# Kernel tuning notes

Hardware: AMD Instinct MI355X
Metric: run time of the kernel (lower is better)

The kernel has to match this reference:

```python
import jax, jax.numpy as jnp
import numpy as np

DIM = 768
N_HEAD = 12
HEAD_DIM = 64
INNER = N_HEAD * HEAD_DIM
SCALE = HEAD_DIM ** -0.5


def setup_inputs() -> dict:
    key = jax.random.key(0)
    ks = jax.random.split(key, 12)
    B, Sf, St = 4, 2048, 2048
    from_tensor = jax.random.normal(ks[0], (B, Sf, DIM), dtype=jnp.float32)
    to_tensor = jax.random.normal(ks[1], (B, St, DIM), dtype=jnp.float32)
    attention_mask = jax.random.randint(ks[2], (B, Sf, St), 0, 2, dtype=jnp.int32)
    # Dense layers: kernel ~ RandomNormal (stddev 0.05, keras default), bias zeros
    def kern(k, fan_in, fan_out):
        return 0.05 * jax.random.normal(k, (fan_in, fan_out), dtype=jnp.float32)
    return {
        "from_tensor": from_tensor,
        "to_tensor": to_tensor,
        "attention_mask": attention_mask,
        "Wq": kern(ks[3], DIM, INNER), "bq": jnp.zeros((INNER,), jnp.float32),
        "Wk": kern(ks[4], DIM, INNER), "bk": jnp.zeros((INNER,), jnp.float32),
        "Wv": kern(ks[5], DIM, INNER), "bv": jnp.zeros((INNER,), jnp.float32),
        "Wo": kern(ks[6], INNER, DIM), "bo": jnp.zeros((DIM,), jnp.float32),
    }


def reference(from_tensor, to_tensor, attention_mask, Wq, bq, Wk, bk, Wv, bv, Wo, bo):
    B, Sf, _ = from_tensor.shape
    St = to_tensor.shape[1]
    # projections -> [B, S, n_head, head_dim] -> [B, n_head, S, head_dim]
    def split_heads(x, S):
        return x.reshape(B, S, N_HEAD, HEAD_DIM).transpose(0, 2, 1, 3)
    q = split_heads(from_tensor @ Wq + bq, Sf) * SCALE
    k = split_heads(to_tensor @ Wk + bk, St)
    v = split_heads(to_tensor @ Wv + bv, St)
    # scores [B, H, Sf, St]
    scores = jnp.einsum('bhik,bhjk->bhij', q, k)
    adder = (1.0 - attention_mask.astype(jnp.float32)) * -10000.0
    scores = scores + adder[:, None, :, :]
    probs = jax.nn.softmax(scores, axis=-1)
    out = jnp.einsum('bhij,bhjk->bhik', probs, v)  # [B, H, Sf, Dh]
    out = out.transpose(0, 2, 1, 3).reshape(B, Sf, INNER)
    return out @ Wo + bo
```

## Files before the change

### kernel.cpp

```cpp
#include <hip/hip_runtime.h>
#include <stdint.h>

#define DIM 768
#define NH 12
#define HD 64
#define BSZ 4
#define SEQ 2048
#define MROWS (BSZ*SEQ)

typedef __attribute__((ext_vector_type(8))) short v8s;
typedef __attribute__((ext_vector_type(4))) float v4f;
typedef __attribute__((ext_vector_type(8))) _Float16 v8h;
typedef __attribute__((ext_vector_type(2))) __fp16 v2fp;

__device__ __forceinline__ uint16_t f2bf(float x) {
  union { float f; uint32_t u; } v; v.f = x;
  uint32_t r = v.u + 0x7fffu + ((v.u >> 16) & 1u);
  return (uint16_t)(r >> 16);
}

#if __has_builtin(__builtin_amdgcn_cvt_pk_bf16_f32)
typedef __attribute__((ext_vector_type(2))) __bf16 v2bf;
__device__ __forceinline__ uint32_t pack_bf16(float a, float b) {
  union { v2bf v; uint32_t u; } c;
  c.v = __builtin_amdgcn_cvt_pk_bf16_f32(a, b);
  return c.u;
}
#else
__device__ __forceinline__ uint32_t pack_bf16(float a, float b) {
  return (uint32_t)f2bf(a) | ((uint32_t)f2bf(b) << 16);
}
#endif

__device__ __forceinline__ uint32_t pack_f16(float a, float b) {
#if __has_builtin(__builtin_amdgcn_cvt_pkrtz)
  union { v2fp h; uint32_t u; } c;
  c.h = __builtin_amdgcn_cvt_pkrtz(a, b);
  return c.u;
#else
  union { _Float16 h[2]; uint32_t u; } c;
  c.h[0] = (_Float16)a; c.h[1] = (_Float16)b; return c.u;
#endif
}

__device__ __forceinline__ float fexp2(float x) {
#if __has_builtin(__builtin_amdgcn_exp2f)
  return __builtin_amdgcn_exp2f(x);
#else
  return exp2f(x);
#endif
}

__device__ __forceinline__ void gl16(const void* g, void* l) {
  __builtin_amdgcn_global_load_lds(
      (const __attribute__((address_space(1))) unsigned int*)g,
      (__attribute__((address_space(3))) unsigned int*)l, 16, 0, 0);
}

__device__ __forceinline__ void pipe_sync() {
  asm volatile("s_waitcnt vmcnt(0)" ::: "memory");
  __builtin_amdgcn_s_barrier();
  __builtin_amdgcn_sched_barrier(0);
}

__global__ void cvt_bf16_kernel(const float* __restrict__ src0, uint16_t* __restrict__ dst0,
                                const float* __restrict__ src1, uint16_t* __restrict__ dst1,
                                int n4) {
  int i = blockIdx.x * blockDim.x + threadIdx.x;
  const float* src = (i < n4) ? src0 : src1;
  uint16_t* dst = (i < n4) ? dst0 : dst1;
  int j = (i < n4) ? i : i - n4;
  float4 v = ((const float4*)src)[j];
  ushort4 o;
  o.x = f2bf(v.x); o.y = f2bf(v.y); o.z = f2bf(v.z); o.w = f2bf(v.w);
  ((ushort4*)dst)[j] = o;
}

__global__ void mask_bits_kernel(const int* __restrict__ src,
                                 unsigned long long* __restrict__ dst, int nwords) {
  int gtid = blockIdx.x * blockDim.x + threadIdx.x;
  int w = gtid >> 6;
  int lane = threadIdx.x & 63;
  if (w >= nwords) return;
  int b  = w >> 16;
  int q  = (w >> 5) & 2047;
  int kt = w & 31;
  int m = src[((size_t)b * SEQ + q) * SEQ + kt * 64 + lane];
  unsigned long long bits = __ballot(m != 0);
  if (lane == 0) dst[((size_t)b * 32 + kt) * SEQ + q] = bits;
}

__global__ void wtrans_kernel(const float* __restrict__ Wq, const float* __restrict__ Wk,
                              const float* __restrict__ Wv, const float* __restrict__ Wo,
                              uint16_t* __restrict__ WT) {
  __shared__ float tile[32][33];
  int z = blockIdx.z;
  const float* src = (z==0) ? Wq : (z==1) ? Wk : (z==2) ? Wv : Wo;
  uint16_t* dst = WT + (size_t)z * DIM * DIM;
  int tx = threadIdx.x, ty = threadIdx.y;
  int x  = blockIdx.x * 32 + tx;
  int y0 = blockIdx.y * 32;
  for (int j = ty; j < 32; j += 8)
    tile[j][tx] = src[(size_t)(y0 + j) * DIM + x];
  __syncthreads();
  int xo = y0 + tx;
  for (int j = ty; j < 32; j += 8)
    dst[(size_t)(blockIdx.x * 32 + j) * DIM + xo] = f2bf(tile[tx][j]);
}

__global__ __launch_bounds__(256) void gemm_kernel(
    const uint16_t* __restrict__ Xf, const uint16_t* __restrict__ Xt,
    const uint16_t* __restrict__ WT, const uint16_t* __restrict__ AO,
    const float* __restrict__ bq, const float* __restrict__ bk,
    const float* __restrict__ bv, const float* __restrict__ bo,
    uint16_t* __restrict__ Qw, uint16_t* __restrict__ Kw, uint16_t* __restrict__ Vw,
    float* __restrict__ Out, int mode_base)
{
  __shared__ alignas(16) uint16_t As[2][128 * 32];
  __shared__ alignas(16) uint16_t Bs[2][128 * 32];
  int mode = mode_base + blockIdx.z;
  const uint16_t* A = (mode == 0) ? Xf : (mode == 3 ? AO : Xt);
  const uint16_t* W = WT + (size_t)mode * DIM * DIM;
  const float* bias = (mode == 0) ? bq : (mode == 1) ? bk : (mode == 2) ? bv : bo;

  int m0 = blockIdx.x * 128, n0 = blockIdx.y * 128;
  int tid = threadIdx.x;
  int wave = tid >> 6, lane = tid & 63, lr = lane & 15, quad = lane >> 4;
  int wm = (wave >> 1) * 64, wn = (wave & 1) * 64;

  int seg = (lane & 3) ^ ((lane >> 3) & 3);
  const uint16_t* agl = A + (size_t)(m0 + wave * 32 + (lane >> 2)) * DIM + seg * 8;
  const uint16_t* bgl = W + (size_t)(n0 + wave * 32 + (lane >> 2)) * DIM + seg * 8;
  int lb = wave * 1024;
  int ck = (lr >> 1) & 3;

  v4f acc[4][4];
  v4f vz = {0.f, 0.f, 0.f, 0.f};
  #pragma unroll
  for (int i = 0; i < 4; i++)
    #pragma unroll
    for (int j = 0; j < 4; j++) acc[i][j] = vz;

  gl16(agl,            &As[0][lb]);
  gl16(agl + 16 * DIM, &As[0][lb + 512]);
  gl16(bgl,            &Bs[0][lb]);
  gl16(bgl + 16 * DIM, &Bs[0][lb + 512]);
  pipe_sync();

  int cur = 0;
  const int NT = DIM / 32;
  for (int t = 0; t < NT; ++t) {
    if (t + 1 < NT) {
      int kn = (t + 1) * 32;
      gl16(agl + kn,            &As[cur ^ 1][lb]);
      gl16(agl + kn + 16 * DIM, &As[cur ^ 1][lb + 512]);
      gl16(bgl + kn,            &Bs[cur ^ 1][lb]);
      gl16(bgl + kn + 16 * DIM, &Bs[cur ^ 1][lb + 512]);
    }
    v8s af[4], bfr[4];
    #pragma unroll
    for (int i = 0; i < 4; i++)
      af[i] = *(const v8s*)&As[cur][(wm + i * 16 + lr) * 32 + ((quad ^ ck) << 3)];
    #pragma unroll
    for (int j = 0; j < 4; j++)
      bfr[j] = *(const v8s*)&Bs[cur][(wn + j * 16 + lr) * 32 + ((quad ^ ck) << 3)];
    #pragma unroll
    for (int i = 0; i < 4; i++)
      #pragma unroll
      for (int j = 0; j < 4; j++)
        acc[i][j] = __builtin_amdgcn_mfma_f32_16x16x32_bf16(af[i], bfr[j], acc[i][j], 0, 0, 0);
    if (t + 1 < NT) pipe_sync();
    cur ^= 1;
  }

  float bj[4];
  #pragma unroll
  for (int j = 0; j < 4; j++) bj[j] = bias[n0 + wn + j * 16 + lr];

  if (mode == 3) {
    #pragma unroll
    for (int i = 0; i < 4; i++) {
      int m = m0 + wm + i * 16 + quad * 4;
      #pragma unroll
      for (int j = 0; j < 4; j++) {
        int n = n0 + wn + j * 16 + lr;
        #pragma unroll
        for (int r = 0; r < 4; r++)
          Out[(size_t)(m + r) * DIM + n] = acc[i][j][r] + bj[j];
      }
    }
  } else if (mode == 2) {
    #pragma unroll
    for (int i = 0; i < 4; i++) {
      int m = m0 + wm + i * 16 + quad * 4;
      int b = m >> 11, s0 = m & 2047;
      int kk0 = s0 & 63;
      int pos = (kk0 >> 5) * 32 + ((kk0 >> 2) & 3) * 8 + ((kk0 >> 4) & 1) * 4;
      int chunk = pos >> 3, off = pos & 7;
      #pragma unroll
      for (int j = 0; j < 4; j++) {
        int n = n0 + wn + j * 16 + lr;
        int h = n >> 6, d = n & 63;
        uint2 pk;
        pk.x = pack_f16(acc[i][j][0] + bj[j], acc[i][j][1] + bj[j]);
        pk.y = pack_f16(acc[i][j][2] + bj[j], acc[i][j][3] + bj[j]);
        int idx = (s0 & ~63) + ((chunk ^ (d & 7)) << 3) + off;
        *(uint2*)&Vw[((size_t)(b * NH + h) * HD + d) * SEQ + idx] = pk;
      }
    }
  } else {
    uint16_t* Dst = (mode == 0) ? Qw : Kw;
    float scale = (mode == 0) ? 0.18033688f : 1.0f;
    #pragma unroll
    for (int i = 0; i < 4; i++) {
      int m = m0 + wm + i * 16 + quad * 4;
      int b = m >> 11, s0 = m & 2047;
      #pragma unroll
      for (int j = 0; j < 4; j++) {
        int n = n0 + wn + j * 16 + lr;
        int h = n >> 6, d = n & 63;
        #pragma unroll
        for (int r = 0; r < 4; r++) {
          float v = (acc[i][j][r] + bj[j]) * scale;
          int s = s0 + r;
          int dd = (mode == 1) ? ((((d >> 3) ^ (s & 7)) << 3) + (d & 7)) : d;
          Dst[((size_t)(b * NH + h) * SEQ + s) * HD + dd] = f2bf(v);
        }
      }
    }
  }
}

__global__ __launch_bounds__(512, 6) void flash_kernel(
    const uint16_t* __restrict__ Qg, const uint16_t* __restrict__ Kg,
    const uint16_t* __restrict__ Vg, const unsigned long long* __restrict__ Mb,
    uint16_t* __restrict__ AO)
{
  __shared__ alignas(16) uint16_t Ks[2][64 * 64];
  __shared__ alignas(16) uint16_t Vs[2][64 * 64];

  int tid = threadIdx.x, wave = tid >> 6, lane = tid & 63, lr = lane & 15, quad = lane >> 4;

  int d = blockIdx.x + (blockIdx.y << 4);
  int nid = (d & 7) * 96 + (d >> 3);
  int bh = nid >> 4;
  int q0 = (nid & 15) * 128;
  int b = bh / NH, h = bh - b * NH;

  const uint16_t* Qp = Qg + (size_t)bh * SEQ * HD;
  const uint16_t* Kp = Kg + (size_t)bh * SEQ * HD;
  const uint16_t* Vp = Vg + (size_t)bh * HD * SEQ;
  int qg = q0 + wave * 16 + lr;
  const unsigned long long* Mp = Mb + (size_t)b * 32 * SEQ + qg;

  int swk = lr & 7, sh0 = quad * 4;

  v8s qfa = *(const v8s*)&Qp[(size_t)qg * HD + quad * 8];
  v8s qfb = *(const v8s*)&Qp[(size_t)qg * HD + 32 + quad * 8];

  const uint16_t* kgl = Kp + ((size_t)(wave * 8 + (lane >> 3)) * HD + (lane & 7) * 8);
  const uint16_t* vgl = Vp + ((size_t)(wave * 8 + (lane >> 3)) * SEQ + (lane & 7) * 8);
  int lb = wave * 512;

  v8h ones;
  #pragma unroll
  for (int i = 0; i < 8; i++) ones[i] = (_Float16)1.0f;

  v4f acc[4], lacc;
  v4f vz = {0.f, 0.f, 0.f, 0.f};
  v4f m8 = {-8.f, -8.f, -8.f, -8.f};
  #pragma unroll
  for (int dt = 0; dt < 4; dt++) acc[dt] = vz;
  lacc = vz;

  gl16(kgl, &Ks[0][lb]);
  gl16(vgl, &Vs[0][lb]);
  unsigned long long mw_cur = Mp[0];
  __syncthreads();

  int cur = 0;
  const int NT = SEQ / 64;
  for (int it = 0; it < NT; ++it) {
    unsigned long long mw_next = 0;
    if (it + 1 < NT) {
      int kn = (it + 1) * 64;
      gl16(kgl + (size_t)kn * HD, &Ks[cur ^ 1][lb]);
      gl16(vgl + kn,              &Vs[cur ^ 1][lb]);
      mw_next = Mp[(size_t)(it + 1) * SEQ];
    }

    uint32_t mlo = (uint32_t)mw_cur, mhi = (uint32_t)(mw_cur >> 32);
    v8h pf[2];
    #pragma unroll
    for (int p = 0; p < 2; p++) {
      v4f sA = m8, sB = m8;
      {
        int rowb = ((2 * p) * 16 + lr) << 6;
        v8s kf0 = *(const v8s*)&Ks[cur][rowb + ((quad ^ swk) << 3)];
        v8s kf1 = *(const v8s*)&Ks[cur][rowb + (((quad + 4) ^ swk) << 3)];
        sA = __builtin_amdgcn_mfma_f32_16x16x32_bf16(kf0, qfa, sA, 0, 0, 0);
        sA = __builtin_amdgcn_mfma_f32_16x16x32_bf16(kf1, qfb, sA, 0, 0, 0);
      }
      {
        int rowb = ((2 * p + 1) * 16 + lr) << 6;
        v8s kf0 = *(const v8s*)&Ks[cur][rowb + ((quad ^ swk) << 3)];
        v8s kf1 = *(const v8s*)&Ks[cur][rowb + (((quad + 4) ^ swk) << 3)];
        sB = __builtin_amdgcn_mfma_f32_16x16x32_bf16(kf0, qfa, sB, 0, 0, 0);
        sB = __builtin_amdgcn_mfma_f32_16x16x32_bf16(kf1, qfb, sB, 0, 0, 0);
      }
      uint32_t mword = p ? mhi : mlo;
      uint32_t b4a = (mword >> sh0) & 15u;
      uint32_t b4b = (mword >> (sh0 + 16)) & 15u;
      float ps[8];
      #pragma unroll
      for (int r = 0; r < 4; r++) {
        float ea = fexp2(sA[r]);
        float eb = fexp2(sB[r]);
        ps[r]     = (b4a & (1u << r)) ? ea : 0.0f;
        ps[4 + r] = (b4b & (1u << r)) ? eb : 0.0f;
      }
      union { uint4 u; v8h h; } cc;
      cc.u.x = pack_f16(ps[0], ps[1]);
      cc.u.y = pack_f16(ps[2], ps[3]);
      cc.u.z = pack_f16(ps[4], ps[5]);
      cc.u.w = pack_f16(ps[6], ps[7]);
      pf[p] = cc.h;
    }

    #pragma unroll
    for (int dt = 0; dt < 4; dt++) {
      int rowb = (dt * 16 + lr) << 6;
      #pragma unroll
      for (int p = 0; p < 2; p++) {
        v8h vv = *(const v8h*)&Vs[cur][rowb + (((p * 4 + quad) ^ swk) << 3)];
        acc[dt] = __builtin_amdgcn_mfma_f32_16x16x32_f16(vv, pf[p], acc[dt], 0, 0, 0);
      }
    }
    lacc = __builtin_amdgcn_mfma_f32_16x16x32_f16(ones, pf[0], lacc, 0, 0, 0);
    lacc = __builtin_amdgcn_mfma_f32_16x16x32_f16(ones, pf[1], lacc, 0, 0, 0);

    __syncthreads();
    mw_cur = mw_next;
    cur ^= 1;
  }

  float ri = 1.0f / lacc[0];

  #pragma unroll
  for (int dt = 0; dt < 4; dt++) {
    uint2 pk;
    pk.x = pack_bf16(acc[dt][0] * ri, acc[dt][1] * ri);
    pk.y = pack_bf16(acc[dt][2] * ri, acc[dt][3] * ri);
    *(uint2*)&AO[(size_t)(b * SEQ + qg) * DIM + h * HD + dt * 16 + sh0] = pk;
  }
}

extern "C" void kernel_launch(void* const* d_in, const int* in_sizes, int n_in,
                              void* d_out, int out_size, void* d_ws, size_t ws_size,
                              hipStream_t stream) {
  const float* from_t = (const float*)d_in[0];
  const float* to_t   = (const float*)d_in[1];
  const int*   maski  = (const int*)d_in[2];
  const float* Wq = (const float*)d_in[3];  const float* bq = (const float*)d_in[4];
  const float* Wk = (const float*)d_in[5];  const float* bk = (const float*)d_in[6];
  const float* Wv = (const float*)d_in[7];  const float* bv = (const float*)d_in[8];
  const float* Wo = (const float*)d_in[9];  const float* bo = (const float*)d_in[10];

  char* ws = (char*)d_ws;
  size_t off = 0;
  uint16_t* Xf = (uint16_t*)(ws + off); off += (size_t)MROWS * DIM * 2;
  uint16_t* Xt = (uint16_t*)(ws + off); off += (size_t)MROWS * DIM * 2;
  uint16_t* WT = (uint16_t*)(ws + off); off += (size_t)4 * DIM * DIM * 2;
  unsigned long long* Mbits = (unsigned long long*)(ws + off);
  off += (size_t)BSZ * 32 * SEQ * 8;
  uint16_t* Qw = (uint16_t*)(ws + off); off += (size_t)MROWS * DIM * 2;
  uint16_t* Kw = (uint16_t*)(ws + off); off += (size_t)MROWS * DIM * 2;
  uint16_t* Vw = (uint16_t*)(ws + off); off += (size_t)MROWS * DIM * 2;
  uint16_t* AO = (uint16_t*)(ws + off); off += (size_t)MROWS * DIM * 2;
  float* Out = (float*)d_out;

  int nx4 = MROWS * DIM / 4;
  cvt_bf16_kernel<<<2 * nx4 / 256, 256, 0, stream>>>(from_t, Xf, to_t, Xt, nx4);
  int nwords = BSZ * 32 * SEQ;
  mask_bits_kernel<<<nwords * 64 / 256, 256, 0, stream>>>(maski, Mbits, nwords);
  wtrans_kernel<<<dim3(24, 24, 4), dim3(32, 8), 0, stream>>>(Wq, Wk, Wv, Wo, WT);

  gemm_kernel<<<dim3(64, 6, 3), 256, 0, stream>>>(Xf, Xt, WT, AO, bq, bk, bv, bo,
                                                  Qw, Kw, Vw, Out, 0);
  flash_kernel<<<dim3(SEQ / 128, BSZ * NH), 512, 0, stream>>>(Qw, Kw, Vw, Mbits, AO);
  gemm_kernel<<<dim3(64, 6, 1), 256, 0, stream>>>(Xf, Xt, WT, AO, bq, bk, bv, bo,
                                                  Qw, Kw, Vw, Out, 3);
}
```

Measured before the change: 328.1 us.

## Fuse prepass kernels into one launch and vectorize GEMM epilogue stores via operand swap

Merges the bf16 conversion, mask bit-packing and weight transpose kernels into a single prepass launch dispatched by block index, which removes two kernel launches and the gaps between them. In the GEMM, the Q/K and output modes swap the MFMA operands so each lane holds four consecutive columns. This lets the epilogue write packed 8-byte bf16 or 16-byte float4 stores and read the bias as a float4, instead of issuing scalar strided stores. The V mode keeps the old operand order and its existing transposed layout.

```diff
diff --git a/kernel.cpp b/kernel.cpp
--- a/kernel.cpp
+++ b/kernel.cpp
@@ -63,49 +63,56 @@
   __builtin_amdgcn_sched_barrier(0);
 }
 
-__global__ void cvt_bf16_kernel(const float* __restrict__ src0, uint16_t* __restrict__ dst0,
-                                const float* __restrict__ src1, uint16_t* __restrict__ dst1,
-                                int n4) {
-  int i = blockIdx.x * blockDim.x + threadIdx.x;
-  const float* src = (i < n4) ? src0 : src1;
-  uint16_t* dst = (i < n4) ? dst0 : dst1;
-  int j = (i < n4) ? i : i - n4;
-  float4 v = ((const float4*)src)[j];
-  ushort4 o;
-  o.x = f2bf(v.x); o.y = f2bf(v.y); o.z = f2bf(v.z); o.w = f2bf(v.w);
-  ((ushort4*)dst)[j] = o;
-}
-
-__global__ void mask_bits_kernel(const int* __restrict__ src,
-                                 unsigned long long* __restrict__ dst, int nwords) {
-  int gtid = blockIdx.x * blockDim.x + threadIdx.x;
-  int w = gtid >> 6;
-  int lane = threadIdx.x & 63;
-  if (w >= nwords) return;
-  int b  = w >> 16;
-  int q  = (w >> 5) & 2047;
-  int kt = w & 31;
-  int m = src[((size_t)b * SEQ + q) * SEQ + kt * 64 + lane];
-  unsigned long long bits = __ballot(m != 0);
-  if (lane == 0) dst[((size_t)b * 32 + kt) * SEQ + q] = bits;
-}
-
-__global__ void wtrans_kernel(const float* __restrict__ Wq, const float* __restrict__ Wk,
-                              const float* __restrict__ Wv, const float* __restrict__ Wo,
-                              uint16_t* __restrict__ WT) {
+#define CVT_BLKS  12288
+#define MASK_BLKS 65536
+#define WT_BLKS   2304
+__global__ __launch_bounds__(256) void prepass_kernel(
+    const float* __restrict__ from_t, const float* __restrict__ to_t,
+    uint16_t* __restrict__ Xf, uint16_t* __restrict__ Xt,
+    const int* __restrict__ maski, unsigned long long* __restrict__ Mbits,
+    const float* __restrict__ Wq, const float* __restrict__ Wk,
+    const float* __restrict__ Wv, const float* __restrict__ Wo,
+    uint16_t* __restrict__ WT)
+{
   __shared__ float tile[32][33];
-  int z = blockIdx.z;
-  const float* src = (z==0) ? Wq : (z==1) ? Wk : (z==2) ? Wv : Wo;
-  uint16_t* dst = WT + (size_t)z * DIM * DIM;
-  int tx = threadIdx.x, ty = threadIdx.y;
-  int x  = blockIdx.x * 32 + tx;
-  int y0 = blockIdx.y * 32;
-  for (int j = ty; j < 32; j += 8)
-    tile[j][tx] = src[(size_t)(y0 + j) * DIM + x];
-  __syncthreads();
-  int xo = y0 + tx;
-  for (int j = ty; j < 32; j += 8)
-    dst[(size_t)(blockIdx.x * 32 + j) * DIM + xo] = f2bf(tile[tx][j]);
+  int blk = blockIdx.x, tid = threadIdx.x;
+  if (blk < CVT_BLKS) {
+    int n4 = MROWS * DIM / 4;
+    int i = blk * 256 + tid;
+    const float* src = (i < n4) ? from_t : to_t;
+    uint16_t* dst = (i < n4) ? Xf : Xt;
+    int j = (i < n4) ? i : i - n4;
+    float4 v = ((const float4*)src)[j];
+    uint2 o;
+    o.x = pack_bf16(v.x, v.y);
+    o.y = pack_bf16(v.z, v.w);
+    ((uint2*)dst)[j] = o;
+  } else if (blk < CVT_BLKS + MASK_BLKS) {
+    int gtid = (blk - CVT_BLKS) * 256 + tid;
+    int w = gtid >> 6;
+    int lane = tid & 63;
+    int b  = w >> 16;
+    int q  = (w >> 5) & 2047;
+    int kt = w & 31;
+    int m = maski[((size_t)b * SEQ + q) * SEQ + kt * 64 + lane];
+    unsigned long long bits = __ballot(m != 0);
+    if (lane == 0) Mbits[((size_t)b * 32 + kt) * SEQ + q] = bits;
+  } else {
+    int r = blk - CVT_BLKS - MASK_BLKS;
+    int z = r / 576, rem = r - z * 576;
+    int by = rem / 24, bx = rem - by * 24;
+    const float* src = (z==0) ? Wq : (z==1) ? Wk : (z==2) ? Wv : Wo;
+    uint16_t* dst = WT + (size_t)z * DIM * DIM;
+    int tx = tid & 31, ty = tid >> 5;
+    int x  = bx * 32 + tx;
+    int y0 = by * 32;
+    for (int jj = ty; jj < 32; jj += 8)
+      tile[jj][tx] = src[(size_t)(y0 + jj) * DIM + x];
+    __syncthreads();
+    int xo = y0 + tx;
+    for (int jj = ty; jj < 32; jj += 8)
+      dst[(size_t)(bx * 32 + jj) * DIM + xo] = f2bf(tile[tx][jj]);
+  }
 }
 
 __global__ __launch_bounds__(256) void gemm_kernel(
@@ -164,32 +171,27 @@
     #pragma unroll
     for (int j = 0; j < 4; j++)
       bfr[j] = *(const v8s*)&Bs[cur][(wn + j * 16 + lr) * 32 + ((quad ^ ck) << 3)];
-    #pragma unroll
-    for (int i = 0; i < 4; i++)
-      #pragma unroll
-      for (int j = 0; j < 4; j++)
-        acc[i][j] = __builtin_amdgcn_mfma_f32_16x16x32_bf16(af[i], bfr[j], acc[i][j], 0, 0, 0);
+    if (mode != 2) {
+      #pragma unroll
+      for (int i = 0; i < 4; i++)
+        #pragma unroll
+        for (int j = 0; j < 4; j++)
+          acc[i][j] = __builtin_amdgcn_mfma_f32_16x16x32_bf16(bfr[j], af[i], acc[i][j], 0, 0, 0);
+    } else {
+      #pragma unroll
+      for (int i = 0; i < 4; i++)
+        #pragma unroll
+        for (int j = 0; j < 4; j++)
+          acc[i][j] = __builtin_amdgcn_mfma_f32_16x16x32_bf16(af[i], bfr[j], acc[i][j], 0, 0, 0);
+    }
     if (t + 1 < NT) pipe_sync();
     cur ^= 1;
   }
 
-  float bj[4];
-  #pragma unroll
-  for (int j = 0; j < 4; j++) bj[j] = bias[n0 + wn + j * 16 + lr];
-
-  if (mode == 3) {
-    #pragma unroll
-    for (int i = 0; i < 4; i++) {
-      int m = m0 + wm + i * 16 + quad * 4;
-      #pragma unroll
-      for (int j = 0; j < 4; j++) {
-        int n = n0 + wn + j * 16 + lr;
-        #pragma unroll
-        for (int r = 0; r < 4; r++)
-          Out[(size_t)(m + r) * DIM + n] = acc[i][j][r] + bj[j];
-      }
-    }
-  } else if (mode == 2) {
+  if (mode == 2) {
+    float bj[4];
+    #pragma unroll
+    for (int j = 0; j < 4; j++) bj[j] = bias[n0 + wn + j * 16 + lr];
     #pragma unroll
     for (int i = 0; i < 4; i++) {
       int m = m0 + wm + i * 16 + quad * 4;
@@ -208,24 +210,43 @@
         *(uint2*)&Vw[((size_t)(b * NH + h) * HD + d) * SEQ + idx] = pk;
       }
     }
+  } else if (mode == 3) {
+    #pragma unroll
+    for (int j = 0; j < 4; j++) {
+      int nb = n0 + wn + j * 16 + quad * 4;
+      float4 b4 = *(const float4*)&bias[nb];
+      #pragma unroll
+      for (int i = 0; i < 4; i++) {
+        int m = m0 + wm + i * 16 + lr;
+        float4 o;
+        o.x = acc[i][j][0] + b4.x;
+        o.y = acc[i][j][1] + b4.y;
+        o.z = acc[i][j][2] + b4.z;
+        o.w = acc[i][j][3] + b4.w;
+        *(float4*)&Out[(size_t)m * DIM + nb] = o;
+      }
+    }
   } else {
     uint16_t* Dst = (mode == 0) ? Qw : Kw;
     float scale = (mode == 0) ? 0.18033688f : 1.0f;
     #pragma unroll
-    for (int i = 0; i < 4; i++) {
-      int m = m0 + wm + i * 16 + quad * 4;
-      int b = m >> 11, s0 = m & 2047;
-      #pragma unroll
-      for (int j = 0; j < 4; j++) {
-        int n = n0 + wn + j * 16 + lr;
-        int h = n >> 6, d = n & 63;
-        #pragma unroll
-        for (int r = 0; r < 4; r++) {
-          float v = (acc[i][j][r] + bj[j]) * scale;
-          int s = s0 + r;
-          int dd = (mode == 1) ? ((((d >> 3) ^ (s & 7)) << 3) + (d & 7)) : d;
-          Dst[((size_t)(b * NH + h) * SEQ + s) * HD + dd] = f2bf(v);
-        }
+    for (int j = 0; j < 4; j++) {
+      int nb = n0 + wn + j * 16 + quad * 4;
+      int h = nb >> 6, d0 = nb & 63;
+      float4 b4 = *(const float4*)&bias[nb];
+      #pragma unroll
+      for (int i = 0; i < 4; i++) {
+        int m = m0 + wm + i * 16 + lr;
+        int b = m >> 11, s = m & 2047;
+        float v0 = (acc[i][j][0] + b4.x) * scale;
+        float v1 = (acc[i][j][1] + b4.y) * scale;
+        float v2 = (acc[i][j][2] + b4.z) * scale;
+        float v3 = (acc[i][j][3] + b4.w) * scale;
+        uint2 pk;
+        pk.x = pack_bf16(v0, v1);
+        pk.y = pack_bf16(v2, v3);
+        int dd = (mode == 1) ? ((((d0 >> 3) ^ (s & 7)) << 3) + (d0 & 7)) : d0;
+        *(uint2*)&Dst[((size_t)(b * NH + h) * SEQ + s) * HD + dd] = pk;
       }
     }
   }
@@ -379,11 +400,8 @@
   uint16_t* AO = (uint16_t*)(ws + off); off += (size_t)MROWS * DIM * 2;
   float* Out = (float*)d_out;
 
-  int nx4 = MROWS * DIM / 4;
-  cvt_bf16_kernel<<<2 * nx4 / 256, 256, 0, stream>>>(from_t, Xf, to_t, Xt, nx4);
-  int nwords = BSZ * 32 * SEQ;
-  mask_bits_kernel<<<nwords * 64 / 256, 256, 0, stream>>>(maski, Mbits, nwords);
-  wtrans_kernel<<<dim3(24, 24, 4), dim3(32, 8), 0, stream>>>(Wq, Wk, Wv, Wo, WT);
+  prepass_kernel<<<CVT_BLKS + MASK_BLKS + WT_BLKS, 256, 0, stream>>>(
+      from_t, to_t, Xf, Xt, maski, Mbits, Wq, Wk, Wv, Wo, WT);
 
   gemm_kernel<<<dim3(64, 6, 3), 256, 0, stream>>>(Xf, Xt, WT, AO, bq, bk, bv, bo,
                                                   Qw, Kw, Vw, Out, 0);
```

After: 395.3 us. +20.5%, slower.
